# Optimization experiments

Measured on AMD Instinct MI355X. Metric: run time of the kernel, lower is better.

Reference implementation:

```python
import jax, jax.numpy as jnp
import numpy as np

HIDDEN = 2304
N_HEADS = 8
N_KV = 4
HEAD_DIM = 256
WINDOW = 1024
SOFTCAP = 50.0
EPS = 1e-6
SCALING = HEAD_DIM ** -0.5  # (head_dim * query_pre_attn_scalar=1.0) ** -0.5


def _rotate_half(x):
    d = x.shape[-1] // 2
    return jnp.concatenate([-x[..., d:], x[..., :d]], axis=-1)


def setup_inputs() -> dict:
    key = jax.random.key(0)
    ks = jax.random.split(key, 8)
    B, S = 2, 2048
    hidden_states = jax.random.normal(ks[0], (B, S, HIDDEN), dtype=jnp.float32)
    # RoPE tables, theta=10000
    inv_freq = 1.0 / (10000.0 ** (jnp.arange(0, HEAD_DIM, 2, dtype=jnp.float32) / HEAD_DIM))
    pos = jnp.arange(S, dtype=jnp.float32)
    freqs = pos[:, None] * inv_freq[None, :]              # [S, D/2]
    emb = jnp.concatenate([freqs, freqs], axis=-1)        # [S, D]
    cos = jnp.broadcast_to(jnp.cos(emb)[None], (B, S, HEAD_DIM)).astype(jnp.float32)
    sin = jnp.broadcast_to(jnp.sin(emb)[None], (B, S, HEAD_DIM)).astype(jnp.float32)
    std = 0.02
    rms_weight = jax.random.normal(ks[1], (HIDDEN,), dtype=jnp.float32) * std
    Wq = jax.random.normal(ks[2], (N_HEADS * HEAD_DIM, HIDDEN), dtype=jnp.float32) * std
    Wk = jax.random.normal(ks[3], (N_KV * HEAD_DIM, HIDDEN), dtype=jnp.float32) * std
    Wv = jax.random.normal(ks[4], (N_KV * HEAD_DIM, HIDDEN), dtype=jnp.float32) * std
    Wo = jax.random.normal(ks[5], (HIDDEN, N_HEADS * HEAD_DIM), dtype=jnp.float32) * std
    return {"hidden_states": hidden_states, "cos": cos, "sin": sin,
            "rms_weight": rms_weight, "Wq": Wq, "Wk": Wk, "Wv": Wv, "Wo": Wo}


def reference(hidden_states, cos, sin, rms_weight, Wq, Wk, Wv, Wo):
    B, S, H = hidden_states.shape
    # Gemma2 RMSNorm: x * rsqrt(mean(x^2)+eps) * (1 + w), computed in fp32
    xf = hidden_states.astype(jnp.float32)
    norm = xf * jax.lax.rsqrt(jnp.mean(xf * xf, axis=-1, keepdims=True) + EPS)
    x = (norm * (1.0 + rms_weight)).astype(hidden_states.dtype)

    q = jnp.einsum('bsh,dh->bsd', x, Wq).reshape(B, S, N_HEADS, HEAD_DIM).transpose(0, 2, 1, 3)
    k = jnp.einsum('bsh,dh->bsd', x, Wk).reshape(B, S, N_KV, HEAD_DIM).transpose(0, 2, 1, 3)
    v = jnp.einsum('bsh,dh->bsd', x, Wv).reshape(B, S, N_KV, HEAD_DIM).transpose(0, 2, 1, 3)

    c = cos[:, None, :, :]  # [B,1,S,D]
    s = sin[:, None, :, :]
    q = q * c + _rotate_half(q) * s
    k = k * c + _rotate_half(k) * s

    groups = N_HEADS // N_KV
    k = jnp.repeat(k, groups, axis=1)  # [B,Hq,S,D]
    v = jnp.repeat(v, groups, axis=1)

    scores = jnp.einsum('bhqd,bhkd->bhqk', q, k) * SCALING
    scores = SOFTCAP * jnp.tanh(scores / SOFTCAP)

    i = jnp.arange(S)[:, None]
    j = jnp.arange(S)[None, :]
    allowed = (j <= i) & ((i - j) < WINDOW)  # causal + sliding window
    scores = jnp.where(allowed[None, None], scores, jnp.float32(-1e30))

    w = jax.nn.softmax(scores.astype(jnp.float32), axis=-1).astype(q.dtype)
    attn = jnp.einsum('bhqk,bhkd->bhqd', w, v)
    attn = attn.transpose(0, 2, 1, 3).reshape(B, S, N_HEADS * HEAD_DIM)
    out = jnp.einsum('bsd,hd->bsh', attn, Wo)
    return hidden_states + out
```

## Files before the change

kernel.cpp:

```cpp
#include <hip/hip_runtime.h>
#include <cstdint>

typedef __bf16 bf16;
typedef __bf16 bf16x8 __attribute__((ext_vector_type(8)));
typedef __bf16 bf16x4 __attribute__((ext_vector_type(4)));
typedef float  f32x4  __attribute__((ext_vector_type(4)));

#define HIDDEN 2304
#define NQ 2048
#define NKV 1024
#define SEQ 2048

typedef __attribute__((address_space(1))) void gv_t;
typedef __attribute__((address_space(3))) void lv_t;
__device__ __forceinline__ void gld16(const void* g, void* l) {
  __builtin_amdgcn_global_load_lds((gv_t*)g, (lv_t*)l, 16, 0, 0);
}

#define BAR()    asm volatile("s_barrier" ::: "memory")
#define LGKM0()  asm volatile("s_waitcnt lgkmcnt(0)" ::: "memory")
#define VM6()    asm volatile("s_waitcnt vmcnt(6)" ::: "memory")
#define VM0()    asm volatile("s_waitcnt vmcnt(0)" ::: "memory")
#define SCHED0() __builtin_amdgcn_sched_barrier(0)

__global__ __launch_bounds__(256) void rmsnorm_kernel(const float* __restrict__ x,
                                                      const float* __restrict__ w,
                                                      bf16* __restrict__ xb) {
  const int row = blockIdx.x, t = threadIdx.x;
  const float* xr = x + (size_t)row * HIDDEN;
  float v[9]; float ss = 0.f;
#pragma unroll
  for (int i = 0; i < 9; ++i) { v[i] = xr[t + i * 256]; ss += v[i] * v[i]; }
#pragma unroll
  for (int o = 32; o; o >>= 1) ss += __shfl_xor(ss, o, 64);
  __shared__ float wss[4];
  if ((t & 63) == 0) wss[t >> 6] = ss;
  __syncthreads();
  ss = wss[0] + wss[1] + wss[2] + wss[3];
  const float rs = rsqrtf(ss * (1.0f / HIDDEN) + 1e-6f);
  bf16* xo = xb + (size_t)row * HIDDEN;
#pragma unroll
  for (int i = 0; i < 9; ++i) xo[t + i * 256] = (bf16)(v[i] * rs * (1.0f + w[t + i * 256]));
}

#define NW0 (2048 * 2304)
#define NW1 (1024 * 2304)
#define NW3 (2304 * 2048)
__global__ __launch_bounds__(256) void cvt4_kernel(const float* __restrict__ s0, const float* __restrict__ s1,
                                                   const float* __restrict__ s2, const float* __restrict__ s3,
                                                   bf16* __restrict__ d0, bf16* __restrict__ d1,
                                                   bf16* __restrict__ d2, bf16* __restrict__ d3) {
  int i = (blockIdx.x * 256 + threadIdx.x) * 4;
  const float* s; bf16* d;
  if (i < NW0) { s = s0; d = d0; }
  else if (i < NW0 + NW1) { s = s1; d = d1; i -= NW0; }
  else if (i < NW0 + 2 * NW1) { s = s2; d = d2; i -= NW0 + NW1; }
  else { s = s3; d = d3; i -= NW0 + 2 * NW1; }
  const float4 f = *(const float4*)(s + i);
  bf16x4 o; o.x = (bf16)f.x; o.y = (bf16)f.y; o.z = (bf16)f.z; o.w = (bf16)f.w;
  *(bf16x4*)(d + i) = o;
}

__global__ __launch_bounds__(256) void rope_kernel(bf16* __restrict__ q, bf16* __restrict__ k,
                                                   const float* __restrict__ cosb,
                                                   const float* __restrict__ sinb) {
  const int tid = blockIdx.x * 256 + threadIdx.x;
  const int QN = 4096 * 8 * 128;
  const int KN = 4096 * 4 * 128;
  bf16* p; int row, d;
  if (tid < QN) {
    row = tid >> 10; const int rem = tid & 1023; d = rem & 127;
    p = q + (size_t)row * NQ + (rem >> 7) * 256 + d;
  } else {
    const int t2 = tid - QN; if (t2 >= KN) return;
    row = t2 >> 9; const int rem = t2 & 511; d = rem & 127;
    p = k + (size_t)row * NKV + (rem >> 7) * 256 + d;
  }
  const size_t cb = (size_t)row * 256 + d;
  const float c0 = cosb[cb], s0 = sinb[cb], c1 = cosb[cb + 128], s1 = sinb[cb + 128];
  const float a = (float)p[0], b = (float)p[128];
  p[0]   = (bf16)(a * c0 - b * s0);
  p[128] = (bf16)(b * c1 + a * s1);
}

__device__ __forceinline__ void stage_half(const char* gbase, int stride, char* ldshalf, int tid) {
  const int c2 = ((tid & 7) * 16) ^ (((tid >> 3) & 7) << 4);
#pragma unroll
  for (int q = 0; q < 2; ++q) {
    const int r = q * 64 + (tid >> 3);
    gld16(gbase + (size_t)r * stride + c2, ldshalf + q * 8192 + tid * 16);
  }
}

template<int MH, int NH>
__device__ __forceinline__ void mfma_cluster(const bf16x8 (&af)[4][2], const bf16x8 (&bn)[2][2],
                                             f32x4 (&acc)[8][4]) {
  __builtin_amdgcn_s_setprio(1);
#pragma unroll
  for (int m = 0; m < 4; ++m)
#pragma unroll
    for (int n = 0; n < 2; ++n) {
      f32x4 c = acc[MH * 4 + m][NH * 2 + n];
      c = __builtin_amdgcn_mfma_f32_16x16x32_bf16(af[m][0], bn[n][0], c, 0, 0, 0);
      c = __builtin_amdgcn_mfma_f32_16x16x32_bf16(af[m][1], bn[n][1], c, 0, 0, 0);
      acc[MH * 4 + m][NH * 2 + n] = c;
    }
  __builtin_amdgcn_s_setprio(0);
}

template<int NT, int NY, int MODE>
__global__ __launch_bounds__(512) void gemm8p(const bf16* __restrict__ A, const bf16* __restrict__ B,
                                              bf16* __restrict__ Cq, bf16* __restrict__ Ck,
                                              bf16* __restrict__ Cvt, float* __restrict__ fo,
                                              const float* __restrict__ resid, int Nd) {
  __shared__ char lds[131072];
  const int Ks = NT * 128;
  const char* Aby = (const char*)A;
  const char* Bby = (const char*)B;

  int wg = blockIdx.x;
  const int chunk = (int)gridDim.x >> 3;
  wg = (wg & 7) * chunk + (wg >> 3);
  const int by = wg % NY, bx = wg / NY;
  const int m0 = bx * 256, n0 = by * 256;

  const int tid = threadIdx.x, lane = tid & 63, wv = tid >> 6;
  const int wm = wv >> 2, wn = wv & 3;
  const int r16 = lane & 15, g = lane >> 4;
  const int xr = (r16 & 7) << 4;
  const int cb0 = (g * 16) ^ xr, cb1 = (64 + g * 16) ^ xr;
  const int rdA = wm * 16384 + r16 * 128;
  const int rdB = 32768 + (wn >> 1) * 16384 + (wn & 1) * 8192 + r16 * 128;

  f32x4 acc[8][4] = {};

  stage_half(Aby + (size_t)m0 * Ks,           Ks, lds + 0,     tid);
  stage_half(Aby + (size_t)(m0 + 128) * Ks,   Ks, lds + 16384, tid);
  stage_half(Bby + (size_t)n0 * Ks,           Ks, lds + 32768, tid);
  stage_half(Bby + (size_t)(n0 + 128) * Ks,   Ks, lds + 49152, tid);
  stage_half(Aby + (size_t)m0 * Ks + 128,         Ks, lds + 65536 + 0,     tid);
  stage_half(Aby + (size_t)(m0 + 128) * Ks + 128, Ks, lds + 65536 + 16384, tid);
  stage_half(Bby + (size_t)n0 * Ks + 128,         Ks, lds + 65536 + 32768, tid);
  VM6(); BAR();

  for (int t = 0; t < NT; ++t) {
    const char* bufc = lds + (size_t)(t & 1) * 65536;
    char* bufn = lds + (size_t)((t + 1) & 1) * 65536;
    char* bufs = lds + (size_t)(t & 1) * 65536;
    bf16x8 a0[4][2], a1[4][2], bb01[2][2], bb23[2][2];
#pragma unroll
    for (int m = 0; m < 4; ++m) {
      a0[m][0] = *(const bf16x8*)(bufc + rdA + m * 2048 + cb0);
      a0[m][1] = *(const bf16x8*)(bufc + rdA + m * 2048 + cb1);
    }
#pragma unroll
    for (int n = 0; n < 2; ++n) {
      bb01[n][0] = *(const bf16x8*)(bufc + rdB + n * 2048 + cb0);
      bb01[n][1] = *(const bf16x8*)(bufc + rdB + n * 2048 + cb1);
    }
    if (t + 1 < NT)
      stage_half(Bby + (size_t)(n0 + 128) * Ks + (size_t)(t + 1) * 128, Ks, bufn + 49152, tid);
    BAR(); LGKM0(); SCHED0();
    mfma_cluster<0, 0>(a0, bb01, acc);
    SCHED0(); BAR();
#pragma unroll
    for (int n = 0; n < 2; ++n) {
      bb23[n][0] = *(const bf16x8*)(bufc + rdB + (2 + n) * 2048 + cb0);
      bb23[n][1] = *(const bf16x8*)(bufc + rdB + (2 + n) * 2048 + cb1);
    }
    BAR(); LGKM0(); SCHED0();
    mfma_cluster<0, 1>(a0, bb23, acc);
    SCHED0(); BAR();
    if (t + 2 < NT)
      stage_half(Aby + (size_t)m0 * Ks + (size_t)(t + 2) * 128, Ks, bufs + 0, tid);
#pragma unroll
    for (int m = 0; m < 4; ++m) {
      a1[m][0] = *(const bf16x8*)(bufc + rdA + 8192 + m * 2048 + cb0);
      a1[m][1] = *(const bf16x8*)(bufc + rdA + 8192 + m * 2048 + cb1);
    }
    BAR(); LGKM0(); SCHED0();
    mfma_cluster<1, 0>(a1, bb01, acc);
    SCHED0(); BAR();
    if (t + 2 < NT) {
      stage_half(Aby + (size_t)(m0 + 128) * Ks + (size_t)(t + 2) * 128, Ks, bufs + 16384, tid);
      stage_half(Bby + (size_t)n0 * Ks + (size_t)(t + 2) * 128, Ks, bufs + 32768, tid);
    }
    if (t < NT - 2) { VM6(); } else if (t == NT - 2) { VM0(); }
    BAR(); SCHED0();
    mfma_cluster<1, 1>(a1, bb23, acc);
    SCHED0(); BAR();
  }

  const int mrow = m0 + wm * 128 + g * 4;
  const int ncol = n0 + wn * 64 + r16;
#pragma unroll
  for (int i = 0; i < 8; ++i)
#pragma unroll
    for (int j = 0; j < 4; ++j)
#pragma unroll
      for (int e = 0; e < 4; ++e) {
        const int m = mrow + i * 16 + e;
        const int n = ncol + j * 16;
        const float vv = acc[i][j][e];
        if constexpr (MODE == 0) {
          if (n0 < 2048) {
            Cq[(size_t)m * 2048 + n] = (bf16)vv;
          } else if (n0 < 3072) {
            Ck[(size_t)m * 1024 + (n - 2048)] = (bf16)vv;
          } else {
            const int b2 = m >> 11, s = m & 2047;
            Cvt[((size_t)b2 * 1024 + (n - 3072)) * SEQ + s] = (bf16)vv;
          }
        } else {
          fo[(size_t)m * Nd + n] = vv + resid[(size_t)m * Nd + n];
        }
      }
}

__device__ __forceinline__ void attn_load(const bf16* __restrict__ kgp, const bf16* __restrict__ vgp,
                                          int j0, int t, bf16x8* kr, bf16x8* vr) {
#pragma unroll
  for (int it = 0; it < 4; ++it) {
    const int flat = it * 2048 + t * 8;
    kr[it] = *(const bf16x8*)&kgp[(size_t)((flat >> 8) + j0) * NKV + (flat & 255)];
    vr[it] = *(const bf16x8*)&vgp[(size_t)(flat >> 5) * SEQ + j0 + (flat & 31)];
  }
}

__global__ __launch_bounds__(256) void attn_kernel(const bf16* __restrict__ q, const bf16* __restrict__ k,
                                                   const bf16* __restrict__ vt, bf16* __restrict__ ao) {
  __shared__ bf16 smem[21248];
  bf16* const qs  = smem;
  bf16* const ksl = smem;
  bf16* const vtl = smem + 8448;
  bf16* const pl  = smem + 18688;
  int qt = blockIdx.x;
  const int h = blockIdx.y, b = blockIdx.z;
  if (b) qt = 31 - qt;
  const int kvh = h >> 1;
  const int t = threadIdx.x, lane = t & 63, w = t >> 6;
  const int r16 = lane & 15, g = lane >> 4;
  const int i_base = qt * 64;

  {
    const bf16* qg = q + ((size_t)(b * SEQ + i_base)) * NQ + h * 256;
#pragma unroll
    for (int it = 0; it < 8; ++it) {
      const int flat = it * 2048 + t * 8;
      const int row = flat >> 8, dd = flat & 255;
      *(bf16x8*)&qs[row * 264 + dd] = *(const bf16x8*)&qg[(size_t)row * NQ + dd];
    }
  }
  __syncthreads();
  bf16x8 aq[8];
#pragma unroll
  for (int c = 0; c < 8; ++c) aq[c] = *(const bf16x8*)&qs[(w * 16 + r16) * 264 + c * 32 + g * 8];

  f32x4 oacc[16] = {};
  float lrun[4] = {0.f, 0.f, 0.f, 0.f};
  int jb = i_base - 1023; if (jb < 0) jb = 0; jb &= ~31;
  const int je = i_base + 63;
  const bf16* kg = k + (size_t)b * SEQ * NKV + kvh * 256;
  const bf16* vg = vt + ((size_t)b * NKV + kvh * 256) * SEQ;

  bf16x8 kr[4], vr[4];
  attn_load(kg, vg, jb, t, kr, vr);

  for (int j0 = jb; j0 <= je; j0 += 32) {
    __syncthreads();
#pragma unroll
    for (int it = 0; it < 4; ++it) {
      const int flat = it * 2048 + t * 8;
      *(bf16x8*)&ksl[(flat >> 8) * 264 + (flat & 255)] = kr[it];
      *(bf16x8*)&vtl[(flat >> 5) * 40 + (flat & 31)] = vr[it];
    }
    __syncthreads();
    const int jn = (j0 + 32 <= je) ? (j0 + 32) : j0;
    attn_load(kg, vg, jn, t, kr, vr);

    f32x4 sc0 = {}, sc1 = {};
#pragma unroll
    for (int c = 0; c < 8; ++c) {
      const bf16x8 b0 = *(const bf16x8*)&ksl[r16 * 264 + c * 32 + g * 8];
      const bf16x8 b1 = *(const bf16x8*)&ksl[(16 + r16) * 264 + c * 32 + g * 8];
      sc0 = __builtin_amdgcn_mfma_f32_16x16x32_bf16(aq[c], b0, sc0, 0, 0, 0);
      sc1 = __builtin_amdgcn_mfma_f32_16x16x32_bf16(aq[c], b1, sc1, 0, 0, 0);
    }
    const bool full = (j0 + 31 <= i_base) && (i_base + 63 - j0 < 1024);
#pragma unroll
    for (int e = 0; e < 4; ++e) {
      const float t0 = __expf(sc0[e] * 0.0025f);
      const float t1 = __expf(sc1[e] * 0.0025f);
      float p0 = __expf(-100.0f / (t0 + 1.0f));
      float p1 = __expf(-100.0f / (t1 + 1.0f));
      if (!full) {
        const int irow = i_base + w * 16 + g * 4 + e;
        const int jg0 = j0 + r16, jg1 = j0 + 16 + r16;
        if (jg0 > irow || irow - jg0 >= 1024) p0 = 0.f;
        if (jg1 > irow || irow - jg1 >= 1024) p1 = 0.f;
      }
      const bf16 b0 = (bf16)p0, b1 = (bf16)p1;
      lrun[e] += (float)b0 + (float)b1;
      pl[w * 640 + (g * 4 + e) * 40 + r16] = b0;
      pl[w * 640 + (g * 4 + e) * 40 + 16 + r16] = b1;
    }
    const bf16x8 pa = *(const bf16x8*)&pl[w * 640 + r16 * 40 + g * 8];
#pragma unroll
    for (int nf = 0; nf < 16; ++nf) {
      const bf16x8 vb = *(const bf16x8*)&vtl[(nf * 16 + r16) * 40 + g * 8];
      oacc[nf] = __builtin_amdgcn_mfma_f32_16x16x32_bf16(pa, vb, oacc[nf], 0, 0, 0);
    }
  }
  float inv[4];
#pragma unroll
  for (int e = 0; e < 4; ++e) {
#pragma unroll
    for (int o = 1; o < 16; o <<= 1) lrun[e] += __shfl_xor(lrun[e], o, 64);
    inv[e] = 1.0f / lrun[e];
  }
  bf16* aor = ao + ((size_t)(b * SEQ + i_base + w * 16)) * NQ + h * 256;
#pragma unroll
  for (int nf = 0; nf < 16; ++nf)
#pragma unroll
    for (int e = 0; e < 4; ++e)
      aor[(size_t)(g * 4 + e) * NQ + nf * 16 + r16] = (bf16)(oacc[nf][e] * inv[e]);
}

extern "C" void kernel_launch(void* const* d_in, const int* in_sizes, int n_in,
                              void* d_out, int out_size, void* d_ws, size_t ws_size,
                              hipStream_t stream) {
  const float* hs   = (const float*)d_in[0];
  const float* cosb = (const float*)d_in[1];
  const float* sinb = (const float*)d_in[2];
  const float* rw   = (const float*)d_in[3];
  const float* Wq   = (const float*)d_in[4];
  const float* Wk   = (const float*)d_in[5];
  const float* Wv   = (const float*)d_in[6];
  const float* Wo   = (const float*)d_in[7];
  float* out = (float*)d_out;
  char* ws = (char*)d_ws;

  bf16* xb   = (bf16*)(ws);
  bf16* wqkv = (bf16*)(ws + 18874368);
  bf16* wkb  = wqkv + (size_t)2048 * 2304;
  bf16* wvb  = wqkv + (size_t)3072 * 2304;
  bf16* wob  = (bf16*)(ws + 37748736);
  bf16* qg   = (bf16*)(ws + 47185920);
  bf16* kg   = (bf16*)(ws + 63963136);
  bf16* vtg  = (bf16*)(ws + 72351744);
  bf16* ag   = (bf16*)(ws + 80740352);

  rmsnorm_kernel<<<4096, 256, 0, stream>>>(hs, rw, xb);
  cvt4_kernel<<<(NW0 + 2 * NW1 + NW3) / 4 / 256, 256, 0, stream>>>(Wq, Wk, Wv, Wo, wqkv, wkb, wvb, wob);
  gemm8p<36, 16, 0><<<256, 512, 0, stream>>>(xb, wqkv, qg, kg, vtg, nullptr, nullptr, 4096);
  rope_kernel<<<(4096 * 8 * 128 + 4096 * 4 * 128) / 256, 256, 0, stream>>>(qg, kg, cosb, sinb);
  attn_kernel<<<dim3(32, 8, 2), 256, 0, stream>>>(qg, kg, vtg, ag);
  gemm8p<32, 9, 1><<<144, 512, 0, stream>>>(ag, wob, nullptr, nullptr, nullptr, out, hs, 2304);
}
```

Measured before the change: 266.7 us.

## Split LDS reads into half-K waits and use smaller-tile GEMM for output projection

The 8-wave GEMM main loop now issues its LDS fragment reads in two K halves. It waits only on the first half (partial lgkmcnt) before starting MFMAs, so the second half of the reads overlaps with compute. All three A/B stage loads for t+2 are also moved together after the third cluster. The output projection switches from 144 large 256x256 tiles to a new simple 128x128 tile kernel with 576 workgroups, so more CUs are busy on the 4096x2304 output. The risks are that the simple kernel has no double-buffering and that the smaller tiles reduce data reuse.

```diff
diff --git a/kernel.cpp b/kernel.cpp
--- a/kernel.cpp
+++ b/kernel.cpp
@@ -18,7 +18,7 @@
 }
 
 #define BAR()    asm volatile("s_barrier" ::: "memory")
-#define LGKM0()  asm volatile("s_waitcnt lgkmcnt(0)" ::: "memory")
+#define LGKM(n)  asm volatile("s_waitcnt lgkmcnt(" #n ")" ::: "memory")
 #define VM6()    asm volatile("s_waitcnt vmcnt(6)" ::: "memory")
 #define VM0()    asm volatile("s_waitcnt vmcnt(0)" ::: "memory")
 #define SCHED0() __builtin_amdgcn_sched_barrier(0)
@@ -92,19 +92,16 @@
   }
 }
 
-template<int MH, int NH>
-__device__ __forceinline__ void mfma_cluster(const bf16x8 (&af)[4][2], const bf16x8 (&bn)[2][2],
-                                             f32x4 (&acc)[8][4]) {
+template<int MH, int NH, int KS>
+__device__ __forceinline__ void mfma_burst(const bf16x8 (&af)[4][2], const bf16x8 (&bn)[2][2],
+                                           f32x4 (&acc)[8][4]) {
   __builtin_amdgcn_s_setprio(1);
 #pragma unroll
   for (int m = 0; m < 4; ++m)
 #pragma unroll
-    for (int n = 0; n < 2; ++n) {
-      f32x4 c = acc[MH * 4 + m][NH * 2 + n];
-      c = __builtin_amdgcn_mfma_f32_16x16x32_bf16(af[m][0], bn[n][0], c, 0, 0, 0);
-      c = __builtin_amdgcn_mfma_f32_16x16x32_bf16(af[m][1], bn[n][1], c, 0, 0, 0);
-      acc[MH * 4 + m][NH * 2 + n] = c;
-    }
+    for (int n = 0; n < 2; ++n)
+      acc[MH * 4 + m][NH * 2 + n] =
+          __builtin_amdgcn_mfma_f32_16x16x32_bf16(af[m][KS], bn[n][KS], acc[MH * 4 + m][NH * 2 + n], 0, 0, 0);
   __builtin_amdgcn_s_setprio(0);
 }
 
@@ -149,45 +146,53 @@
     char* bufs = lds + (size_t)(t & 1) * 65536;
     bf16x8 a0[4][2], a1[4][2], bb01[2][2], bb23[2][2];
 #pragma unroll
-    for (int m = 0; m < 4; ++m) {
-      a0[m][0] = *(const bf16x8*)(bufc + rdA + m * 2048 + cb0);
-      a0[m][1] = *(const bf16x8*)(bufc + rdA + m * 2048 + cb1);
-    }
-#pragma unroll
-    for (int n = 0; n < 2; ++n) {
-      bb01[n][0] = *(const bf16x8*)(bufc + rdB + n * 2048 + cb0);
-      bb01[n][1] = *(const bf16x8*)(bufc + rdB + n * 2048 + cb1);
-    }
+    for (int n = 0; n < 2; ++n) bb01[n][0] = *(const bf16x8*)(bufc + rdB + n * 2048 + cb0);
+#pragma unroll
+    for (int m = 0; m < 4; ++m) a0[m][0] = *(const bf16x8*)(bufc + rdA + m * 2048 + cb0);
+    SCHED0();
+#pragma unroll
+    for (int n = 0; n < 2; ++n) bb01[n][1] = *(const bf16x8*)(bufc + rdB + n * 2048 + cb1);
+#pragma unroll
+    for (int m = 0; m < 4; ++m) a0[m][1] = *(const bf16x8*)(bufc + rdA + m * 2048 + cb1);
     if (t + 1 < NT)
       stage_half(Bby + (size_t)(n0 + 128) * Ks + (size_t)(t + 1) * 128, Ks, bufn + 49152, tid);
-    BAR(); LGKM0(); SCHED0();
-    mfma_cluster<0, 0>(a0, bb01, acc);
+    BAR();
+    LGKM(6); SCHED0();
+    mfma_burst<0, 0, 0>(a0, bb01, acc);
+    SCHED0(); LGKM(0); SCHED0();
+    mfma_burst<0, 0, 1>(a0, bb01, acc);
     SCHED0(); BAR();
 #pragma unroll
-    for (int n = 0; n < 2; ++n) {
-      bb23[n][0] = *(const bf16x8*)(bufc + rdB + (2 + n) * 2048 + cb0);
-      bb23[n][1] = *(const bf16x8*)(bufc + rdB + (2 + n) * 2048 + cb1);
-    }
-    BAR(); LGKM0(); SCHED0();
-    mfma_cluster<0, 1>(a0, bb23, acc);
+    for (int n = 0; n < 2; ++n) bb23[n][0] = *(const bf16x8*)(bufc + rdB + (2 + n) * 2048 + cb0);
+    SCHED0();
+#pragma unroll
+    for (int n = 0; n < 2; ++n) bb23[n][1] = *(const bf16x8*)(bufc + rdB + (2 + n) * 2048 + cb1);
+    BAR();
+    LGKM(2); SCHED0();
+    mfma_burst<0, 1, 0>(a0, bb23, acc);
+    SCHED0(); LGKM(0); SCHED0();
+    mfma_burst<0, 1, 1>(a0, bb23, acc);
     SCHED0(); BAR();
-    if (t + 2 < NT)
-      stage_half(Aby + (size_t)m0 * Ks + (size_t)(t + 2) * 128, Ks, bufs + 0, tid);
-#pragma unroll
-    for (int m = 0; m < 4; ++m) {
-      a1[m][0] = *(const bf16x8*)(bufc + rdA + 8192 + m * 2048 + cb0);
-      a1[m][1] = *(const bf16x8*)(bufc + rdA + 8192 + m * 2048 + cb1);
-    }
-    BAR(); LGKM0(); SCHED0();
-    mfma_cluster<1, 0>(a1, bb01, acc);
+#pragma unroll
+    for (int m = 0; m < 4; ++m) a1[m][0] = *(const bf16x8*)(bufc + rdA + 8192 + m * 2048 + cb0);
+    SCHED0();
+#pragma unroll
+    for (int m = 0; m < 4; ++m) a1[m][1] = *(const bf16x8*)(bufc + rdA + 8192 + m * 2048 + cb1);
+    BAR();
+    LGKM(4); SCHED0();
+    mfma_burst<1, 0, 0>(a1, bb01, acc);
+    SCHED0(); LGKM(0); SCHED0();
+    mfma_burst<1, 0, 1>(a1, bb01, acc);
     SCHED0(); BAR();
     if (t + 2 < NT) {
-      stage_half(Aby + (size_t)(m0 + 128) * Ks + (size_t)(t + 2) * 128, Ks, bufs + 16384, tid);
-      stage_half(Bby + (size_t)n0 * Ks + (size_t)(t + 2) * 128, Ks, bufs + 32768, tid);
+      stage_half(Aby + (size_t)m0 * Ks + (size_t)(t + 2) * 128,           Ks, bufs + 0,     tid);
+      stage_half(Aby + (size_t)(m0 + 128) * Ks + (size_t)(t + 2) * 128,   Ks, bufs + 16384, tid);
+      stage_half(Bby + (size_t)n0 * Ks + (size_t)(t + 2) * 128,           Ks, bufs + 32768, tid);
     }
     if (t < NT - 2) { VM6(); } else if (t == NT - 2) { VM0(); }
     BAR(); SCHED0();
-    mfma_cluster<1, 1>(a1, bb23, acc);
+    mfma_burst<1, 1, 0>(a1, bb23, acc);
+    mfma_burst<1, 1, 1>(a1, bb23, acc);
     SCHED0(); BAR();
   }
 
@@ -217,6 +222,57 @@
       }
 }
 
+template<int KD>
+__global__ __launch_bounds__(256) void gemm2p(const bf16* __restrict__ A, const bf16* __restrict__ B,
+                                              float* __restrict__ fo, const float* __restrict__ resid) {
+  __shared__ bf16 As[128 * 64];
+  __shared__ bf16 Bs[128 * 64];
+  const int t = threadIdx.x, lane = t & 63, w = t >> 6;
+  const int wr = w >> 1, wc = w & 1;
+  const int r16 = lane & 15, g = lane >> 4;
+  int wg = blockIdx.x;
+  const int chunk = (int)gridDim.x >> 3;
+  wg = (wg & 7) * chunk + (wg >> 3);
+  const int bx = wg / 18, by = wg % 18;
+  const int m0 = bx * 128, n0 = by * 128;
+  f32x4 acc[4][4] = {};
+  for (int k0 = 0; k0 < KD; k0 += 64) {
+    __syncthreads();
+#pragma unroll
+    for (int c = 0; c < 4; ++c) {
+      const int o = c * 4096 + t * 16;
+      const int row = o >> 7, col = (o & 127) >> 1;
+      gld16(&A[(size_t)(m0 + row) * KD + k0 + col], (char*)As + o);
+      gld16(&B[(size_t)(n0 + row) * KD + k0 + col], (char*)Bs + o);
+    }
+    __syncthreads();
+#pragma unroll
+    for (int ks = 0; ks < 2; ++ks) {
+      bf16x8 af[4], bfv[4];
+#pragma unroll
+      for (int i = 0; i < 4; ++i) {
+        af[i]  = *(const bf16x8*)&As[(wr * 64 + i * 16 + r16) * 64 + ks * 32 + g * 8];
+        bfv[i] = *(const bf16x8*)&Bs[(wc * 64 + i * 16 + r16) * 64 + ks * 32 + g * 8];
+      }
+#pragma unroll
+      for (int i = 0; i < 4; ++i)
+#pragma unroll
+        for (int j = 0; j < 4; ++j)
+          acc[i][j] = __builtin_amdgcn_mfma_f32_16x16x32_bf16(af[i], bfv[j], acc[i][j], 0, 0, 0);
+    }
+  }
+#pragma unroll
+  for (int i = 0; i < 4; ++i)
+#pragma unroll
+    for (int j = 0; j < 4; ++j) {
+      const int mb = m0 + wr * 64 + i * 16 + g * 4;
+      const int n = n0 + wc * 64 + j * 16 + r16;
+#pragma unroll
+      for (int e = 0; e < 4; ++e)
+        fo[(size_t)(mb + e) * 2304 + n] = acc[i][j][e] + resid[(size_t)(mb + e) * 2304 + n];
+    }
+}
+
 __device__ __forceinline__ void attn_load(const bf16* __restrict__ kgp, const bf16* __restrict__ vgp,
                                           int j0, int t, bf16x8* kr, bf16x8* vr) {
 #pragma unroll
@@ -355,5 +411,5 @@
   gemm8p<36, 16, 0><<<256, 512, 0, stream>>>(xb, wqkv, qg, kg, vtg, nullptr, nullptr, 4096);
   rope_kernel<<<(4096 * 8 * 128 + 4096 * 4 * 128) / 256, 256, 0, stream>>>(qg, kg, cosb, sinb);
   attn_kernel<<<dim3(32, 8, 2), 256, 0, stream>>>(qg, kg, vtg, ag);
-  gemm8p<32, 9, 1><<<144, 512, 0, stream>>>(ag, wob, nullptr, nullptr, nullptr, out, hs, 2304);
-}
+  gemm2p<2048><<<576, 256, 0, stream>>>(ag, wob, out, hs);
+}
```

After: 294.1 us. 10.3% more time.
